# Performance work log

Hardware: AMD Instinct MI355X
Metric: run time of the kernel (lower is better)

The kernel has to match this reference:

```python
import jax, jax.numpy as jnp
import numpy as np

N, E, D, DE, H = 50000, 400000, 128, 64, 8
EPS = 1e-5
SLOPE = 0.2


def setup_inputs() -> dict:
    key = jax.random.key(0)
    ks = jax.random.split(key, 16)

    def lin(k, fan_in, fan_out):
        return (jax.random.normal(k, (fan_in, fan_out), jnp.float32) / np.sqrt(fan_in)).astype(jnp.float32)

    return {
        "node_features": jax.random.normal(ks[0], (N, D), jnp.float32),
        "edge_features": jax.random.normal(ks[1], (E, DE), jnp.float32),
        "Wn": lin(ks[2], D, D), "bn": jnp.zeros((D,), jnp.float32),
        "Wq": lin(ks[3], D, D), "bq": jnp.zeros((D,), jnp.float32),
        "Wk": lin(ks[4], D, D), "bk": jnp.zeros((D,), jnp.float32),
        "Wv": lin(ks[5], D, D), "bv": jnp.zeros((D,), jnp.float32),
        "We": lin(ks[6], DE, D), "be": jnp.zeros((D,), jnp.float32),
        "A1": lin(ks[7], 3 * D, D), "b1": jnp.zeros((D,), jnp.float32),
        "A2": lin(ks[8], D, H), "b2": jnp.zeros((H,), jnp.float32),
        "gamma": jnp.ones((D,), jnp.float32),
        "beta": jnp.zeros((D,), jnp.float32),
        "edge_index": jax.random.randint(ks[9], (2, E), 0, N, dtype=jnp.int32),
    }


def reference(node_features, edge_features, Wn, bn, Wq, bq, Wk, bk, Wv, bv,
              We, be, A1, b1, A2, b2, gamma, beta, edge_index):
    num_nodes = node_features.shape[0]
    h = node_features @ Wn + bn                      # [N, D]
    q = node_features @ Wq + bq                      # [N, D]
    k = node_features @ Wk + bk                      # [N, D]
    v = node_features @ Wv + bv                      # [N, D]
    eh = edge_features @ We + be                     # [E, D]

    src, tgt = edge_index[0], edge_index[1]
    attn_in = jnp.concatenate([q[src], k[tgt], eh], axis=-1)   # [E, 3D]
    hmid = jax.nn.leaky_relu(attn_in @ A1 + b1, SLOPE)          # [E, D]
    scores = jax.nn.leaky_relu(hmid @ A2 + b2, SLOPE)           # [E, H]
    w = jax.nn.softmax(scores.mean(axis=-1), axis=0)            # global softmax over edges, [E]

    # scatter-add: output[src] += w * v[tgt]
    out = jax.ops.segment_sum(w[:, None] * v[tgt], src, num_segments=num_nodes)  # [N, D]

    y = h + out                                       # dropout = identity (eval)
    mu = y.mean(axis=-1, keepdims=True)
    var = y.var(axis=-1, keepdims=True)
    return gamma * (y - mu) / jnp.sqrt(var + EPS) + beta
```

## Files before the change

### kernel.cpp

```cpp
#include <hip/hip_runtime.h>

#define D 128
#define DE 64
#define SLOPE 0.2f
#define EPS 1e-5f

typedef float f32x4 __attribute__((ext_vector_type(4)));
typedef short bf16x8 __attribute__((ext_vector_type(8)));
typedef unsigned short ushort;

__device__ __forceinline__ float lrelu(float x) { return x > 0.f ? x : SLOPE * x; }

__device__ __forceinline__ ushort f2bf(float x) {
  union { float f; unsigned u; } c; c.f = x;
  unsigned r = c.u + 0x7FFFu + ((c.u >> 16) & 1u);
  return (ushort)(r >> 16);
}
__device__ __forceinline__ float bf2f(unsigned u) {
  return __uint_as_float(u << 16);
}

__global__ __launch_bounds__(128) void fold_pack(
    const float* __restrict__ Wq, const float* __restrict__ Wk,
    const float* __restrict__ We, const float* __restrict__ A1,
    const float* __restrict__ bq, const float* __restrict__ bk,
    const float* __restrict__ be, const float* __restrict__ b1,
    const float* __restrict__ Wn, const float* __restrict__ Wv,
    ushort* __restrict__ AfqT, ushort* __restrict__ AfkT,
    ushort* __restrict__ AfeT, float* __restrict__ bfold,
    ushort* __restrict__ WnT, ushort* __restrict__ WvT) {
  int r = blockIdx.x;
  int j = threadIdx.x;
  if (r < 128) {
    float acc = 0.f;
    for (int t = 0; t < 128; ++t) acc += Wq[r * 128 + t] * A1[t * 128 + j];
    AfqT[j * 128 + r] = f2bf(acc);
  } else if (r < 256) {
    int k = r - 128;
    float acc = 0.f;
    for (int t = 0; t < 128; ++t) acc += Wk[k * 128 + t] * A1[(128 + t) * 128 + j];
    AfkT[j * 128 + k] = f2bf(acc);
  } else if (r < 320) {
    int k = r - 256;
    float acc = 0.f;
    for (int t = 0; t < 128; ++t) acc += We[k * 128 + t] * A1[(256 + t) * 128 + j];
    AfeT[j * 64 + k] = f2bf(acc);
  } else if (r == 320) {
    float acc = b1[j];
    for (int t = 0; t < 128; ++t) {
      acc += bq[t] * A1[t * 128 + j];
      acc += bk[t] * A1[(128 + t) * 128 + j];
      acc += be[t] * A1[(256 + t) * 128 + j];
    }
    bfold[j] = acc;
  } else if (r < 449) {
    int c = r - 321;
    WnT[c * 128 + j] = f2bf(Wn[j * 128 + c]);
  } else {
    int c = r - 449;
    WvT[c * 128 + j] = f2bf(Wv[j * 128 + c]);
  }
}

__global__ __launch_bounds__(256) void cvt_count(
    const float* __restrict__ X, ushort* __restrict__ Xb, int n4,
    const int* __restrict__ src, int* __restrict__ deg, int E) {
  int i = blockIdx.x * 256 + threadIdx.x;
  if (i < n4) {
    float4 f = ((const float4*)X)[i];
    union { ushort us[4]; uint2 v; } u;
    u.us[0] = f2bf(f.x); u.us[1] = f2bf(f.y);
    u.us[2] = f2bf(f.z); u.us[3] = f2bf(f.w);
    ((uint2*)Xb)[i] = u.v;
  }
  if (i < E) atomicAdd(&deg[src[i]], 1);
}

__global__ __launch_bounds__(256, 2) void node_gemm_mfma(
    const ushort* __restrict__ Xb, const ushort* __restrict__ WnT,
    const ushort* __restrict__ WvT, const ushort* __restrict__ AfqT,
    const ushort* __restrict__ AfkT, const float* __restrict__ bn,
    const float* __restrict__ bv, float* __restrict__ h,
    ushort* __restrict__ vb, ushort* __restrict__ q2p,
    ushort* __restrict__ k2p, int Nn) {
  __shared__ ushort As[256 * 40];
  __shared__ ushort Bs[128 * 40];
  __shared__ float bS[128];
  const ushort* WT;
  const float* bb = nullptr;
  float* O = nullptr;
  ushort* Ob = nullptr;
  int mode;
  switch (blockIdx.y) {
    case 0: WT = WnT; bb = bn; O = h; mode = 0; break;
    case 1: WT = WvT; bb = bv; Ob = vb; mode = 1; break;
    case 2: WT = AfqT; Ob = q2p; mode = 2; break;
    default: WT = AfkT; Ob = k2p; mode = 2; break;
  }
  const int t = threadIdx.x;
  if (t < 128) bS[t] = bb ? bb[t] : 0.f;
  const int seg = t & 3, arow = t >> 2;
  const int m0 = blockIdx.x * 256;
  int rIdx[4];
#pragma unroll
  for (int l = 0; l < 4; ++l) rIdx[l] = min(m0 + arow + 64 * l, Nn - 1);
  uint4 avA[4], avB[2];
#pragma unroll
  for (int l = 0; l < 4; ++l)
    avA[l] = *(const uint4*)(Xb + (size_t)rIdx[l] * 128 + seg * 8);
#pragma unroll
  for (int l = 0; l < 2; ++l)
    avB[l] = *(const uint4*)(WT + (arow + 64 * l) * 128 + seg * 8);
  f32x4 acc[4][8];
#pragma unroll
  for (int mt = 0; mt < 4; ++mt)
#pragma unroll
    for (int nt = 0; nt < 8; ++nt) acc[mt][nt] = (f32x4)(0.f);
  const int lane = t & 63, wv = t >> 6, l15 = lane & 15, quad = lane >> 4;
  for (int ch = 0; ch < 4; ++ch) {
#pragma unroll
    for (int l = 0; l < 4; ++l)
      *(uint4*)&As[(arow + 64 * l) * 40 + seg * 8] = avA[l];
#pragma unroll
    for (int l = 0; l < 2; ++l)
      *(uint4*)&Bs[(arow + 64 * l) * 40 + seg * 8] = avB[l];
    __syncthreads();
    if (ch < 3) {
      int o = (ch + 1) * 32 + seg * 8;
#pragma unroll
      for (int l = 0; l < 4; ++l)
        avA[l] = *(const uint4*)(Xb + (size_t)rIdx[l] * 128 + o);
#pragma unroll
      for (int l = 0; l < 2; ++l)
        avB[l] = *(const uint4*)(WT + (arow + 64 * l) * 128 + o);
    }
    bf16x8 af[4];
#pragma unroll
    for (int mt = 0; mt < 4; ++mt)
      af[mt] = *(const bf16x8*)&As[(wv * 64 + mt * 16 + l15) * 40 + quad * 8];
#pragma unroll
    for (int nt = 0; nt < 8; ++nt) {
      bf16x8 bfr = *(const bf16x8*)&Bs[(nt * 16 + l15) * 40 + quad * 8];
#pragma unroll
      for (int mt = 0; mt < 4; ++mt)
        acc[mt][nt] =
            __builtin_amdgcn_mfma_f32_16x16x32_bf16(af[mt], bfr, acc[mt][nt], 0, 0, 0);
    }
    __syncthreads();
  }
#pragma unroll
  for (int mt = 0; mt < 4; ++mt) {
    int rowb = m0 + wv * 64 + mt * 16 + quad * 4;
#pragma unroll
    for (int nt = 0; nt < 8; ++nt) {
      int col = nt * 16 + l15;
      float b = bS[col];
#pragma unroll
      for (int r = 0; r < 4; ++r) {
        int rg = rowb + r;
        if (rg < Nn) {
          if (mode == 0)      O[(size_t)rg * 128 + col] = acc[mt][nt][r] + b;
          else if (mode == 1) Ob[(size_t)rg * 128 + col] = f2bf(acc[mt][nt][r] + b);
          else                Ob[(size_t)rg * 128 + l15 * 8 + nt] = f2bf(acc[mt][nt][r]);
        }
      }
    }
  }
}

__global__ __launch_bounds__(256, 2) void edge_fused3(
    const float* __restrict__ EF, const ushort* __restrict__ AfeT,
    const float* __restrict__ bfold, const float* __restrict__ A2,
    const float* __restrict__ b2, const ushort* __restrict__ q2p,
    const ushort* __restrict__ k2p, const int* __restrict__ src,
    const int* __restrict__ tgt, float* __restrict__ s_out, int E) {
  __shared__ ushort As[256 * 40];
  __shared__ ushort Bs[128 * 40];
  __shared__ float A2s[128 * 9];
  __shared__ float bfS[128];
  __shared__ float b2s[8];
  const int t = threadIdx.x;
  const int e0 = blockIdx.x * 256;
  const int lane = t & 63, wv = t >> 6, l15 = lane & 15, quad = lane >> 4;

  int siA[16], tiA[16];
#pragma unroll
  for (int mt = 0; mt < 4; ++mt)
#pragma unroll
    for (int r = 0; r < 4; ++r) {
      int e = min(e0 + wv * 64 + mt * 16 + quad * 4 + r, E - 1);
      siA[mt * 4 + r] = src[e];
      tiA[mt * 4 + r] = tgt[e];
    }
  {
    if (t < 128) bfS[t] = bfold[t];
    if (t < 8) b2s[t] = b2[t];
#pragma unroll
    for (int l = 0; l < 4; ++l) {
      int i = t + l * 256;
      A2s[(i >> 3) * 9 + (i & 7)] = A2[i];
    }
  }
  const int seg = t & 3, arow = t >> 2;
  int ecl[4];
#pragma unroll
  for (int l = 0; l < 4; ++l) ecl[l] = min(e0 + arow + 64 * l, E - 1);
  uint4 avA[4], avB[2];
#pragma unroll
  for (int l = 0; l < 4; ++l) {
    const float* p = EF + (size_t)ecl[l] * 64 + seg * 8;
    float4 f0 = *(const float4*)p;
    float4 f1 = *(const float4*)(p + 4);
    union { ushort us[8]; uint4 v; } u;
    u.us[0] = f2bf(f0.x); u.us[1] = f2bf(f0.y);
    u.us[2] = f2bf(f0.z); u.us[3] = f2bf(f0.w);
    u.us[4] = f2bf(f1.x); u.us[5] = f2bf(f1.y);
    u.us[6] = f2bf(f1.z); u.us[7] = f2bf(f1.w);
    avA[l] = u.v;
  }
#pragma unroll
  for (int l = 0; l < 2; ++l)
    avB[l] = *(const uint4*)(AfeT + (arow + 64 * l) * 64 + seg * 8);
  f32x4 acc[4][8];
#pragma unroll
  for (int mt = 0; mt < 4; ++mt)
#pragma unroll
    for (int nt = 0; nt < 8; ++nt) acc[mt][nt] = (f32x4)(0.f);

#pragma unroll
  for (int ch = 0; ch < 2; ++ch) {
#pragma unroll
    for (int l = 0; l < 4; ++l)
      *(uint4*)&As[(arow + 64 * l) * 40 + seg * 8] = avA[l];
#pragma unroll
    for (int l = 0; l < 2; ++l)
      *(uint4*)&Bs[(arow + 64 * l) * 40 + seg * 8] = avB[l];
    __syncthreads();
    if (ch == 0) {
      int o = 32 + seg * 8;
#pragma unroll
      for (int l = 0; l < 4; ++l) {
        const float* p = EF + (size_t)ecl[l] * 64 + o;
        float4 f0 = *(const float4*)p;
        float4 f1 = *(const float4*)(p + 4);
        union { ushort us[8]; uint4 v; } u;
        u.us[0] = f2bf(f0.x); u.us[1] = f2bf(f0.y);
        u.us[2] = f2bf(f0.z); u.us[3] = f2bf(f0.w);
        u.us[4] = f2bf(f1.x); u.us[5] = f2bf(f1.y);
        u.us[6] = f2bf(f1.z); u.us[7] = f2bf(f1.w);
        avA[l] = u.v;
      }
#pragma unroll
      for (int l = 0; l < 2; ++l)
        avB[l] = *(const uint4*)(AfeT + (arow + 64 * l) * 64 + o);
    }
    bf16x8 af[4];
#pragma unroll
    for (int mt = 0; mt < 4; ++mt)
      af[mt] = *(const bf16x8*)&As[(wv * 64 + mt * 16 + l15) * 40 + quad * 8];
#pragma unroll
    for (int nt = 0; nt < 8; ++nt) {
      bf16x8 bfr = *(const bf16x8*)&Bs[(nt * 16 + l15) * 40 + quad * 8];
#pragma unroll
      for (int mt = 0; mt < 4; ++mt)
        acc[mt][nt] =
            __builtin_amdgcn_mfma_f32_16x16x32_bf16(af[mt], bfr, acc[mt][nt], 0, 0, 0);
    }
    if (ch == 0) __syncthreads();
  }

  float bfv[8];
#pragma unroll
  for (int nt = 0; nt < 8; ++nt) bfv[nt] = bfS[nt * 16 + l15];
  uint4 qv[2][4], kv[2][4];
#pragma unroll
  for (int r = 0; r < 4; ++r) {
    qv[0][r] = *(const uint4*)(q2p + (size_t)siA[r] * 128 + l15 * 8);
    kv[0][r] = *(const uint4*)(k2p + (size_t)tiA[r] * 128 + l15 * 8);
  }
#pragma unroll
  for (int mt = 0; mt < 4; ++mt) {
    int cur = mt & 1;
    if (mt < 3) {
#pragma unroll
      for (int r = 0; r < 4; ++r) {
        qv[cur ^ 1][r] = *(const uint4*)(q2p + (size_t)siA[(mt + 1) * 4 + r] * 128 + l15 * 8);
        kv[cur ^ 1][r] = *(const uint4*)(k2p + (size_t)tiA[(mt + 1) * 4 + r] * 128 + l15 * 8);
      }
    }
#pragma unroll
    for (int r = 0; r < 4; ++r) {
      const ushort* qs = (const ushort*)&qv[cur][r];
      const ushort* ks = (const ushort*)&kv[cur][r];
#pragma unroll
      for (int nt = 0; nt < 8; ++nt)
        acc[mt][nt][r] =
            lrelu(acc[mt][nt][r] + bf2f(qs[nt]) + bf2f(ks[nt]) + bfv[nt]);
    }
  }
  float tacc[4][4];
#pragma unroll
  for (int mt = 0; mt < 4; ++mt)
#pragma unroll
    for (int r = 0; r < 4; ++r) tacc[mt][r] = 0.f;
  for (int hh = 0; hh < 8; ++hh) {
    float a2v[8];
#pragma unroll
    for (int nt = 0; nt < 8; ++nt) a2v[nt] = A2s[nt * 144 + l15 * 9 + hh];
    float b2h = b2s[hh];
#pragma unroll
    for (int mt = 0; mt < 4; ++mt)
#pragma unroll
      for (int r = 0; r < 4; ++r) {
        float p = 0.f;
#pragma unroll
        for (int nt = 0; nt < 8; ++nt) p += acc[mt][nt][r] * a2v[nt];
        p += __shfl_xor(p, 1);
        p += __shfl_xor(p, 2);
        p += __shfl_xor(p, 4);
        p += __shfl_xor(p, 8);
        tacc[mt][r] += lrelu(p + b2h);
      }
  }
  if (l15 == 0) {
#pragma unroll
    for (int mt = 0; mt < 4; ++mt)
#pragma unroll
      for (int r = 0; r < 4; ++r) {
        int e = e0 + wv * 64 + mt * 16 + quad * 4 + r;
        if (e < E) s_out[e] = tacc[mt][r] * 0.125f;
      }
  }
}

__global__ __launch_bounds__(256) void softmax_partial(
    const float* __restrict__ s, int E, float2* __restrict__ part) {
  __shared__ float mS[256], sS[256];
  int tid = threadIdx.x;
  float m = -1e30f, sum = 0.f;
  for (int i = blockIdx.x * 256 + tid; i < E; i += gridDim.x * 256) {
    float x = s[i];
    if (x > m) {
      sum = sum * __expf(m - x) + 1.f;
      m = x;
    } else {
      sum += __expf(x - m);
    }
  }
  mS[tid] = m;
  sS[tid] = sum;
  __syncthreads();
  for (int off = 128; off > 0; off >>= 1) {
    if (tid < off) {
      float m1 = mS[tid], s1 = sS[tid];
      float m2 = mS[tid + off], s2 = sS[tid + off];
      float M = fmaxf(m1, m2);
      mS[tid] = M;
      sS[tid] = s1 * __expf(m1 - M) + s2 * __expf(m2 - M);
    }
    __syncthreads();
  }
  if (tid == 0) part[blockIdx.x] = make_float2(mS[0], sS[0]);
}

__global__ __launch_bounds__(256) void softmax_final(
    const float2* __restrict__ part, int nPart, float* __restrict__ MS) {
  __shared__ float mS[256], sS[256];
  int tid = threadIdx.x;
  float m = -1e30f, sum = 0.f;
  for (int i = tid; i < nPart; i += 256) {
    float2 p = part[i];
    float M = fmaxf(m, p.x);
    sum = sum * __expf(m - M) + p.y * __expf(p.x - M);
    m = M;
  }
  mS[tid] = m;
  sS[tid] = sum;
  __syncthreads();
  for (int off = 128; off > 0; off >>= 1) {
    if (tid < off) {
      float m1 = mS[tid], s1 = sS[tid];
      float m2 = mS[tid + off], s2 = sS[tid + off];
      float M = fmaxf(m1, m2);
      mS[tid] = M;
      sS[tid] = s1 * __expf(m1 - M) + s2 * __expf(m2 - M);
    }
    __syncthreads();
  }
  if (tid == 0) {
    MS[0] = mS[0];
    MS[1] = 1.f / sS[0];
  }
}

__global__ __launch_bounds__(256) void scan1(const int* __restrict__ deg,
                                             int* __restrict__ incl,
                                             int* __restrict__ bsum, int N) {
  __shared__ int sh[256];
  int tid = threadIdx.x;
  int i = blockIdx.x * 256 + tid;
  sh[tid] = (i < N) ? deg[i] : 0;
  __syncthreads();
  for (int off = 1; off < 256; off <<= 1) {
    int tv = (tid >= off) ? sh[tid - off] : 0;
    __syncthreads();
    sh[tid] += tv;
    __syncthreads();
  }
  if (i < N) incl[i] = sh[tid];
  if (tid == 255) bsum[blockIdx.x] = sh[255];
}

__global__ __launch_bounds__(256) void scan2(int* __restrict__ bsum, int nb) {
  __shared__ int sh[256];
  int tid = threadIdx.x;
  sh[tid] = (tid < nb) ? bsum[tid] : 0;
  __syncthreads();
  for (int off = 1; off < 256; off <<= 1) {
    int tv = (tid >= off) ? sh[tid - off] : 0;
    __syncthreads();
    sh[tid] += tv;
    __syncthreads();
  }
  if (tid < nb) bsum[tid] = sh[tid];
}

__global__ __launch_bounds__(256) void scan3(const int* __restrict__ deg,
                                             const int* __restrict__ incl,
                                             const int* __restrict__ bsum,
                                             int* __restrict__ offs,
                                             int* __restrict__ cursor, int N,
                                             int E) {
  int i = blockIdx.x * 256 + threadIdx.x;
  if (i >= N) return;
  int base = (blockIdx.x > 0) ? bsum[blockIdx.x - 1] : 0;
  int ex = incl[i] - deg[i] + base;
  offs[i] = ex;
  cursor[i] = ex;
  if (i == N - 1) offs[N] = E;
}

__global__ __launch_bounds__(256) void fill_csr(
    const int* __restrict__ src, const int* __restrict__ tgt,
    const float* __restrict__ s, int* __restrict__ cursor,
    int2* __restrict__ cwt, int E) {
  int e = blockIdx.x * 256 + threadIdx.x;
  if (e >= E) return;
  int s_ = src[e];
  int j = atomicAdd(&cursor[s_], 1);
  cwt[j] = make_int2(tgt[e], __float_as_int(s[e]));
}

__global__ __launch_bounds__(256) void gather_ln(
    const int* __restrict__ offs, const int2* __restrict__ cwt,
    const ushort* __restrict__ vb, const float* __restrict__ MS,
    const float* __restrict__ gamma, const float* __restrict__ beta,
    float* __restrict__ y, int N) {
  int tid = threadIdx.x;
  int n = blockIdx.x * 4 + (tid >> 6);
  if (n >= N) return;
  int lane = tid & 63;
  float M = MS[0], inv = MS[1];
  int beg = offs[n], end = offs[n + 1];
  float a0 = 0.f, a1 = 0.f;
  int j = beg;
  for (; j + 1 < end; j += 2) {
    int2 p0 = cwt[j], p1 = cwt[j + 1];
    float w0 = __expf(__int_as_float(p0.y) - M) * inv;
    float w1 = __expf(__int_as_float(p1.y) - M) * inv;
    unsigned u0 = *(const unsigned*)(vb + (size_t)p0.x * 128 + lane * 2);
    unsigned u1 = *(const unsigned*)(vb + (size_t)p1.x * 128 + lane * 2);
    a0 += w0 * bf2f(u0 & 0xffffu) + w1 * bf2f(u1 & 0xffffu);
    a1 += w0 * bf2f(u0 >> 16) + w1 * bf2f(u1 >> 16);
  }
  if (j < end) {
    int2 p = cwt[j];
    float w = __expf(__int_as_float(p.y) - M) * inv;
    unsigned u = *(const unsigned*)(vb + (size_t)p.x * 128 + lane * 2);
    a0 += w * bf2f(u & 0xffffu);
    a1 += w * bf2f(u >> 16);
  }
  size_t base = (size_t)n * 128 + lane * 2;
  float2 hv = *(const float2*)(y + base);
  float y0 = hv.x + a0, y1 = hv.y + a1;
  float sum = y0 + y1, ssq = y0 * y0 + y1 * y1;
#pragma unroll
  for (int off = 1; off < 64; off <<= 1) {
    sum += __shfl_xor(sum, off);
    ssq += __shfl_xor(ssq, off);
  }
  float mu = sum * (1.f / 128.f);
  float var = ssq * (1.f / 128.f) - mu * mu;
  float rstd = rsqrtf(var + EPS);
  float2 g = *(const float2*)(gamma + lane * 2);
  float2 bt = *(const float2*)(beta + lane * 2);
  float2 out;
  out.x = g.x * (y0 - mu) * rstd + bt.x;
  out.y = g.y * (y1 - mu) * rstd + bt.y;
  *(float2*)(y + base) = out;
}

extern "C" void kernel_launch(void* const* d_in, const int* in_sizes, int n_in,
                              void* d_out, int out_size, void* d_ws,
                              size_t ws_size, hipStream_t stream) {
  const float* X  = (const float*)d_in[0];
  const float* EF = (const float*)d_in[1];
  const float* Wn = (const float*)d_in[2];
  const float* bn = (const float*)d_in[3];
  const float* Wq = (const float*)d_in[4];
  const float* bq = (const float*)d_in[5];
  const float* Wk = (const float*)d_in[6];
  const float* bk = (const float*)d_in[7];
  const float* Wv = (const float*)d_in[8];
  const float* bv = (const float*)d_in[9];
  const float* We = (const float*)d_in[10];
  const float* be = (const float*)d_in[11];
  const float* A1 = (const float*)d_in[12];
  const float* b1 = (const float*)d_in[13];
  const float* A2 = (const float*)d_in[14];
  const float* b2 = (const float*)d_in[15];
  const float* gamma = (const float*)d_in[16];
  const float* beta  = (const float*)d_in[17];
  const int* ei = (const int*)d_in[18];

  int N = in_sizes[0] / D;
  int E = in_sizes[1] / DE;
  const int* src = ei;
  const int* tgt = ei + E;

  float* h = (float*)d_out;
  float* ws = (float*)d_ws;
  float* sbuf  = ws;
  float2* part = (float2*)(sbuf + E);
  float* MS    = (float*)(part + 1024);
  float* bfold = MS + 4;
  ushort* Xb   = (ushort*)(bfold + 128);
  ushort* vb   = Xb + (size_t)N * D;
  ushort* q2p  = vb + (size_t)N * D;
  ushort* k2p  = q2p + (size_t)N * D;
  ushort* AfqT = k2p + (size_t)N * D;
  ushort* AfkT = AfqT + 128 * 128;
  ushort* AfeT = AfkT + 128 * 128;
  ushort* WnT  = AfeT + 128 * 64;
  ushort* WvT  = WnT + 128 * 128;
  int* deg    = (int*)(WvT + 128 * 128);
  int* incl   = deg + N;
  int* bsum   = incl + N;
  int* cursor = bsum + 256;
  int* offs   = cursor + N;
  int2* cwt   = (int2*)(offs + N + 2);

  int nbScan = (N + 255) / 256;
  int n4 = N * D / 4;

  hipMemsetAsync(deg, 0, (size_t)N * sizeof(int), stream);
  fold_pack<<<577, 128, 0, stream>>>(Wq, Wk, We, A1, bq, bk, be, b1, Wn, Wv,
                                     AfqT, AfkT, AfeT, bfold, WnT, WvT);
  cvt_count<<<(n4 + 255) / 256, 256, 0, stream>>>(X, Xb, n4, src, deg, E);
  scan1<<<nbScan, 256, 0, stream>>>(deg, incl, bsum, N);
  scan2<<<1, 256, 0, stream>>>(bsum, nbScan);
  scan3<<<nbScan, 256, 0, stream>>>(deg, incl, bsum, offs, cursor, N, E);
  node_gemm_mfma<<<dim3((N + 255) / 256, 4), 256, 0, stream>>>(
      Xb, WnT, WvT, AfqT, AfkT, bn, bv, h, vb, q2p, k2p, N);
  edge_fused3<<<(E + 255) / 256, 256, 0, stream>>>(EF, AfeT, bfold, A2, b2,
                                                   q2p, k2p, src, tgt, sbuf, E);
  softmax_partial<<<1024, 256, 0, stream>>>(sbuf, E, part);
  softmax_final<<<1, 256, 0, stream>>>(part, 1024, MS);
  fill_csr<<<(E + 255) / 256, 256, 0, stream>>>(src, tgt, sbuf, cursor, cwt, E);
  gather_ln<<<(N + 3) / 4, 256, 0, stream>>>(offs, cwt, vb, MS, gamma, beta, h,
                                             N);
}
```

Measured before the change: 457.3 us.

## Fuse X conversion into node GEMM and softmax/CSR fill into edge kernel

After: 384.6 us. 1.19x faster.

```diff
diff --git a/kernel.cpp b/kernel.cpp
--- a/kernel.cpp
+++ b/kernel.cpp
@@ -18,6 +18,16 @@
 }
 __device__ __forceinline__ float bf2f(unsigned u) {
   return __uint_as_float(u << 16);
+}
+__device__ __forceinline__ uint4 cvt8(const float* p) {
+  float4 f0 = *(const float4*)p;
+  float4 f1 = *(const float4*)(p + 4);
+  union { ushort us[8]; uint4 v; } u;
+  u.us[0] = f2bf(f0.x); u.us[1] = f2bf(f0.y);
+  u.us[2] = f2bf(f0.z); u.us[3] = f2bf(f0.w);
+  u.us[4] = f2bf(f1.x); u.us[5] = f2bf(f1.y);
+  u.us[6] = f2bf(f1.z); u.us[7] = f2bf(f1.w);
+  return u.v;
 }
 
 __global__ __launch_bounds__(128) void fold_pack(
@@ -28,7 +38,8 @@
     const float* __restrict__ Wn, const float* __restrict__ Wv,
     ushort* __restrict__ AfqT, ushort* __restrict__ AfkT,
     ushort* __restrict__ AfeT, float* __restrict__ bfold,
-    ushort* __restrict__ WnT, ushort* __restrict__ WvT) {
+    ushort* __restrict__ WnT, ushort* __restrict__ WvT,
+    const int* __restrict__ src, int* __restrict__ deg, int E) {
   int r = blockIdx.x;
   int j = threadIdx.x;
   if (r < 128) {
@@ -56,28 +67,17 @@
   } else if (r < 449) {
     int c = r - 321;
     WnT[c * 128 + j] = f2bf(Wn[j * 128 + c]);
-  } else {
+  } else if (r < 577) {
     int c = r - 449;
     WvT[c * 128 + j] = f2bf(Wv[j * 128 + c]);
-  }
-}
-
-__global__ __launch_bounds__(256) void cvt_count(
-    const float* __restrict__ X, ushort* __restrict__ Xb, int n4,
-    const int* __restrict__ src, int* __restrict__ deg, int E) {
-  int i = blockIdx.x * 256 + threadIdx.x;
-  if (i < n4) {
-    float4 f = ((const float4*)X)[i];
-    union { ushort us[4]; uint2 v; } u;
-    u.us[0] = f2bf(f.x); u.us[1] = f2bf(f.y);
-    u.us[2] = f2bf(f.z); u.us[3] = f2bf(f.w);
-    ((uint2*)Xb)[i] = u.v;
-  }
-  if (i < E) atomicAdd(&deg[src[i]], 1);
+  } else {
+    int i = (r - 577) * 128 + j;
+    if (i < E) atomicAdd(&deg[src[i]], 1);
+  }
 }
 
 __global__ __launch_bounds__(256, 2) void node_gemm_mfma(
-    const ushort* __restrict__ Xb, const ushort* __restrict__ WnT,
+    const float* __restrict__ X, const ushort* __restrict__ WnT,
     const ushort* __restrict__ WvT, const ushort* __restrict__ AfqT,
     const ushort* __restrict__ AfkT, const float* __restrict__ bn,
     const float* __restrict__ bv, float* __restrict__ h,
@@ -107,7 +107,7 @@
   uint4 avA[4], avB[2];
 #pragma unroll
   for (int l = 0; l < 4; ++l)
-    avA[l] = *(const uint4*)(Xb + (size_t)rIdx[l] * 128 + seg * 8);
+    avA[l] = cvt8(X + (size_t)rIdx[l] * 128 + seg * 8);
 #pragma unroll
   for (int l = 0; l < 2; ++l)
     avB[l] = *(const uint4*)(WT + (arow + 64 * l) * 128 + seg * 8);
@@ -129,7 +129,7 @@
       int o = (ch + 1) * 32 + seg * 8;
 #pragma unroll
       for (int l = 0; l < 4; ++l)
-        avA[l] = *(const uint4*)(Xb + (size_t)rIdx[l] * 128 + o);
+        avA[l] = cvt8(X + (size_t)rIdx[l] * 128 + o);
 #pragma unroll
       for (int l = 0; l < 2; ++l)
         avB[l] = *(const uint4*)(WT + (arow + 64 * l) * 128 + o);
@@ -168,101 +168,76 @@
   }
 }
 
-__global__ __launch_bounds__(256, 2) void edge_fused3(
+__global__ __launch_bounds__(256, 3) void edge_fused4(
     const float* __restrict__ EF, const ushort* __restrict__ AfeT,
     const float* __restrict__ bfold, const float* __restrict__ A2,
     const float* __restrict__ b2, const ushort* __restrict__ q2p,
     const ushort* __restrict__ k2p, const int* __restrict__ src,
-    const int* __restrict__ tgt, float* __restrict__ s_out, int E) {
-  __shared__ ushort As[256 * 40];
+    const int* __restrict__ tgt, int* __restrict__ cursor,
+    int2* __restrict__ cwt, float2* __restrict__ part, int E) {
+  __shared__ ushort As[128 * 40];
   __shared__ ushort Bs[128 * 40];
   __shared__ float A2s[128 * 9];
   __shared__ float bfS[128];
   __shared__ float b2s[8];
+  __shared__ int sIdxS[128], sIdxT[128];
+  __shared__ float redM[16], redS[16];
   const int t = threadIdx.x;
-  const int e0 = blockIdx.x * 256;
+  const int e0 = blockIdx.x * 128;
+  if (t < 128) {
+    sIdxS[t] = src[min(e0 + t, E - 1)];
+    bfS[t] = bfold[t];
+  } else {
+    sIdxT[t - 128] = tgt[min(e0 + t - 128, E - 1)];
+  }
+  if (t < 8) b2s[t] = b2[t];
+#pragma unroll
+  for (int l = 0; l < 4; ++l) {
+    int i = t + l * 256;
+    A2s[(i >> 3) * 9 + (i & 7)] = A2[i];
+  }
+  const int seg = t & 3, arow = t >> 2;
+  int ecl[2];
+#pragma unroll
+  for (int l = 0; l < 2; ++l) ecl[l] = min(e0 + arow + 64 * l, E - 1);
+  uint4 avA[2], avB[2];
+#pragma unroll
+  for (int l = 0; l < 2; ++l) {
+    avA[l] = cvt8(EF + (size_t)ecl[l] * 64 + seg * 8);
+    avB[l] = *(const uint4*)(AfeT + (arow + 64 * l) * 64 + seg * 8);
+  }
+  f32x4 acc[2][8];
+#pragma unroll
+  for (int mt = 0; mt < 2; ++mt)
+#pragma unroll
+    for (int nt = 0; nt < 8; ++nt) acc[mt][nt] = (f32x4)(0.f);
   const int lane = t & 63, wv = t >> 6, l15 = lane & 15, quad = lane >> 4;
 
-  int siA[16], tiA[16];
-#pragma unroll
-  for (int mt = 0; mt < 4; ++mt)
-#pragma unroll
-    for (int r = 0; r < 4; ++r) {
-      int e = min(e0 + wv * 64 + mt * 16 + quad * 4 + r, E - 1);
-      siA[mt * 4 + r] = src[e];
-      tiA[mt * 4 + r] = tgt[e];
-    }
-  {
-    if (t < 128) bfS[t] = bfold[t];
-    if (t < 8) b2s[t] = b2[t];
-#pragma unroll
-    for (int l = 0; l < 4; ++l) {
-      int i = t + l * 256;
-      A2s[(i >> 3) * 9 + (i & 7)] = A2[i];
-    }
-  }
-  const int seg = t & 3, arow = t >> 2;
-  int ecl[4];
-#pragma unroll
-  for (int l = 0; l < 4; ++l) ecl[l] = min(e0 + arow + 64 * l, E - 1);
-  uint4 avA[4], avB[2];
-#pragma unroll
-  for (int l = 0; l < 4; ++l) {
-    const float* p = EF + (size_t)ecl[l] * 64 + seg * 8;
-    float4 f0 = *(const float4*)p;
-    float4 f1 = *(const float4*)(p + 4);
-    union { ushort us[8]; uint4 v; } u;
-    u.us[0] = f2bf(f0.x); u.us[1] = f2bf(f0.y);
-    u.us[2] = f2bf(f0.z); u.us[3] = f2bf(f0.w);
-    u.us[4] = f2bf(f1.x); u.us[5] = f2bf(f1.y);
-    u.us[6] = f2bf(f1.z); u.us[7] = f2bf(f1.w);
-    avA[l] = u.v;
-  }
-#pragma unroll
-  for (int l = 0; l < 2; ++l)
-    avB[l] = *(const uint4*)(AfeT + (arow + 64 * l) * 64 + seg * 8);
-  f32x4 acc[4][8];
-#pragma unroll
-  for (int mt = 0; mt < 4; ++mt)
-#pragma unroll
-    for (int nt = 0; nt < 8; ++nt) acc[mt][nt] = (f32x4)(0.f);
-
 #pragma unroll
   for (int ch = 0; ch < 2; ++ch) {
 #pragma unroll
-    for (int l = 0; l < 4; ++l)
+    for (int l = 0; l < 2; ++l) {
       *(uint4*)&As[(arow + 64 * l) * 40 + seg * 8] = avA[l];
-#pragma unroll
-    for (int l = 0; l < 2; ++l)
       *(uint4*)&Bs[(arow + 64 * l) * 40 + seg * 8] = avB[l];
+    }
     __syncthreads();
     if (ch == 0) {
       int o = 32 + seg * 8;
 #pragma unroll
-      for (int l = 0; l < 4; ++l) {
-        const float* p = EF + (size_t)ecl[l] * 64 + o;
-        float4 f0 = *(const float4*)p;
-        float4 f1 = *(const float4*)(p + 4);
-        union { ushort us[8]; uint4 v; } u;
-        u.us[0] = f2bf(f0.x); u.us[1] = f2bf(f0.y);
-        u.us[2] = f2bf(f0.z); u.us[3] = f2bf(f0.w);
-        u.us[4] = f2bf(f1.x); u.us[5] = f2bf(f1.y);
-        u.us[6] = f2bf(f1.z); u.us[7] = f2bf(f1.w);
-        avA[l] = u.v;
+      for (int l = 0; l < 2; ++l) {
+        avA[l] = cvt8(EF + (size_t)ecl[l] * 64 + o);
+        avB[l] = *(const uint4*)(AfeT + (arow + 64 * l) * 64 + o);
       }
-#pragma unroll
-      for (int l = 0; l < 2; ++l)
-        avB[l] = *(const uint4*)(AfeT + (arow + 64 * l) * 64 + o);
-    }
-    bf16x8 af[4];
-#pragma unroll
-    for (int mt = 0; mt < 4; ++mt)
-      af[mt] = *(const bf16x8*)&As[(wv * 64 + mt * 16 + l15) * 40 + quad * 8];
+    }
+    bf16x8 af[2];
+#pragma unroll
+    for (int mt = 0; mt < 2; ++mt)
+      af[mt] = *(const bf16x8*)&As[(wv * 32 + mt * 16 + l15) * 40 + quad * 8];
 #pragma unroll
     for (int nt = 0; nt < 8; ++nt) {
       bf16x8 bfr = *(const bf16x8*)&Bs[(nt * 16 + l15) * 40 + quad * 8];
 #pragma unroll
-      for (int mt = 0; mt < 4; ++mt)
+      for (int mt = 0; mt < 2; ++mt)
         acc[mt][nt] =
             __builtin_amdgcn_mfma_f32_16x16x32_bf16(af[mt], bfr, acc[mt][nt], 0, 0, 0);
     }
@@ -272,35 +247,25 @@
   float bfv[8];
 #pragma unroll
   for (int nt = 0; nt < 8; ++nt) bfv[nt] = bfS[nt * 16 + l15];
-  uint4 qv[2][4], kv[2][4];
-#pragma unroll
-  for (int r = 0; r < 4; ++r) {
-    qv[0][r] = *(const uint4*)(q2p + (size_t)siA[r] * 128 + l15 * 8);
-    kv[0][r] = *(const uint4*)(k2p + (size_t)tiA[r] * 128 + l15 * 8);
-  }
-#pragma unroll
-  for (int mt = 0; mt < 4; ++mt) {
-    int cur = mt & 1;
-    if (mt < 3) {
-#pragma unroll
-      for (int r = 0; r < 4; ++r) {
-        qv[cur ^ 1][r] = *(const uint4*)(q2p + (size_t)siA[(mt + 1) * 4 + r] * 128 + l15 * 8);
-        kv[cur ^ 1][r] = *(const uint4*)(k2p + (size_t)tiA[(mt + 1) * 4 + r] * 128 + l15 * 8);
-      }
-    }
+#pragma unroll
+  for (int mt = 0; mt < 2; ++mt) {
 #pragma unroll
     for (int r = 0; r < 4; ++r) {
-      const ushort* qs = (const ushort*)&qv[cur][r];
-      const ushort* ks = (const ushort*)&kv[cur][r];
+      int erow = wv * 32 + mt * 16 + quad * 4 + r;
+      int si = sIdxS[erow], ti = sIdxT[erow];
+      uint4 qv = *(const uint4*)(q2p + (size_t)si * 128 + l15 * 8);
+      uint4 kv = *(const uint4*)(k2p + (size_t)ti * 128 + l15 * 8);
+      const ushort* qs = (const ushort*)&qv;
+      const ushort* ks = (const ushort*)&kv;
 #pragma unroll
       for (int nt = 0; nt < 8; ++nt)
         acc[mt][nt][r] =
             lrelu(acc[mt][nt][r] + bf2f(qs[nt]) + bf2f(ks[nt]) + bfv[nt]);
     }
   }
-  float tacc[4][4];
-#pragma unroll
-  for (int mt = 0; mt < 4; ++mt)
+  float tacc[2][4];
+#pragma unroll
+  for (int mt = 0; mt < 2; ++mt)
 #pragma unroll
     for (int r = 0; r < 4; ++r) tacc[mt][r] = 0.f;
   for (int hh = 0; hh < 8; ++hh) {
@@ -309,7 +274,7 @@
     for (int nt = 0; nt < 8; ++nt) a2v[nt] = A2s[nt * 144 + l15 * 9 + hh];
     float b2h = b2s[hh];
 #pragma unroll
-    for (int mt = 0; mt < 4; ++mt)
+    for (int mt = 0; mt < 2; ++mt)
 #pragma unroll
       for (int r = 0; r < 4; ++r) {
         float p = 0.f;
@@ -323,44 +288,46 @@
       }
   }
   if (l15 == 0) {
-#pragma unroll
-    for (int mt = 0; mt < 4; ++mt)
+    float sc[8];
+    float m = -1e30f;
+#pragma unroll
+    for (int mt = 0; mt < 2; ++mt)
 #pragma unroll
       for (int r = 0; r < 4; ++r) {
-        int e = e0 + wv * 64 + mt * 16 + quad * 4 + r;
-        if (e < E) s_out[e] = tacc[mt][r] * 0.125f;
+        int i = mt * 4 + r;
+        sc[i] = tacc[mt][r] * 0.125f;
+        int e = e0 + wv * 32 + mt * 16 + quad * 4 + r;
+        if (e < E) m = fmaxf(m, sc[i]);
       }
-  }
-}
-
-__global__ __launch_bounds__(256) void softmax_partial(
-    const float* __restrict__ s, int E, float2* __restrict__ part) {
-  __shared__ float mS[256], sS[256];
-  int tid = threadIdx.x;
-  float m = -1e30f, sum = 0.f;
-  for (int i = blockIdx.x * 256 + tid; i < E; i += gridDim.x * 256) {
-    float x = s[i];
-    if (x > m) {
-      sum = sum * __expf(m - x) + 1.f;
-      m = x;
-    } else {
-      sum += __expf(x - m);
-    }
-  }
-  mS[tid] = m;
-  sS[tid] = sum;
+    float ssum = 0.f;
+#pragma unroll
+    for (int mt = 0; mt < 2; ++mt)
+#pragma unroll
+      for (int r = 0; r < 4; ++r) {
+        int i = mt * 4 + r;
+        int erow = wv * 32 + mt * 16 + quad * 4 + r;
+        if (e0 + erow < E) {
+          ssum += __expf(sc[i] - m);
+          int j = atomicAdd(&cursor[sIdxS[erow]], 1);
+          cwt[j] = make_int2(sIdxT[erow], __float_as_int(sc[i]));
+        }
+      }
+    int rid = wv * 4 + quad;
+    redM[rid] = m;
+    redS[rid] = ssum;
+  }
   __syncthreads();
-  for (int off = 128; off > 0; off >>= 1) {
-    if (tid < off) {
-      float m1 = mS[tid], s1 = sS[tid];
-      float m2 = mS[tid + off], s2 = sS[tid + off];
-      float M = fmaxf(m1, m2);
-      mS[tid] = M;
-      sS[tid] = s1 * __expf(m1 - M) + s2 * __expf(m2 - M);
-    }
-    __syncthreads();
-  }
-  if (tid == 0) part[blockIdx.x] = make_float2(mS[0], sS[0]);
+  if (t == 0) {
+    float M = redM[0], S = redS[0];
+#pragma unroll
+    for (int i = 1; i < 16; ++i) {
+      float m2 = redM[i], s2 = redS[i];
+      float Mn = fmaxf(M, m2);
+      S = S * __expf(M - Mn) + s2 * __expf(m2 - Mn);
+      M = Mn;
+    }
+    part[blockIdx.x] = make_float2(M, S);
+  }
 }
 
 __global__ __launch_bounds__(256) void softmax_final(
@@ -440,17 +407,6 @@
   if (i == N - 1) offs[N] = E;
 }
 
-__global__ __launch_bounds__(256) void fill_csr(
-    const int* __restrict__ src, const int* __restrict__ tgt,
-    const float* __restrict__ s, int* __restrict__ cursor,
-    int2* __restrict__ cwt, int E) {
-  int e = blockIdx.x * 256 + threadIdx.x;
-  if (e >= E) return;
-  int s_ = src[e];
-  int j = atomicAdd(&cursor[s_], 1);
-  cwt[j] = make_int2(tgt[e], __float_as_int(s[e]));
-}
-
 __global__ __launch_bounds__(256) void gather_ln(
     const int* __restrict__ offs, const int2* __restrict__ cwt,
     const ushort* __restrict__ vb, const float* __restrict__ MS,
@@ -464,16 +420,22 @@
   int beg = offs[n], end = offs[n + 1];
   float a0 = 0.f, a1 = 0.f;
   int j = beg;
-  for (; j + 1 < end; j += 2) {
-    int2 p0 = cwt[j], p1 = cwt[j + 1];
+  for (; j + 4 <= end; j += 4) {
+    int2 p0 = cwt[j], p1 = cwt[j + 1], p2 = cwt[j + 2], p3 = cwt[j + 3];
+    unsigned u0 = *(const unsigned*)(vb + (size_t)p0.x * 128 + lane * 2);
+    unsigned u1 = *(const unsigned*)(vb + (size_t)p1.x * 128 + lane * 2);
+    unsigned u2 = *(const unsigned*)(vb + (size_t)p2.x * 128 + lane * 2);
+    unsigned u3 = *(const unsigned*)(vb + (size_t)p3.x * 128 + lane * 2);
     float w0 = __expf(__int_as_float(p0.y) - M) * inv;
     float w1 = __expf(__int_as_float(p1.y) - M) * inv;
-    unsigned u0 = *(const unsigned*)(vb + (size_t)p0.x * 128 + lane * 2);
-    unsigned u1 = *(const unsigned*)(vb + (size_t)p1.x * 128 + lane * 2);
-    a0 += w0 * bf2f(u0 & 0xffffu) + w1 * bf2f(u1 & 0xffffu);
-    a1 += w0 * bf2f(u0 >> 16) + w1 * bf2f(u1 >> 16);
-  }
-  if (j < end) {
+    float w2 = __expf(__int_as_float(p2.y) - M) * inv;
+    float w3 = __expf(__int_as_float(p3.y) - M) * inv;
+    a0 += w0 * bf2f(u0 & 0xffffu) + w1 * bf2f(u1 & 0xffffu) +
+          w2 * bf2f(u2 & 0xffffu) + w3 * bf2f(u3 & 0xffffu);
+    a1 += w0 * bf2f(u0 >> 16) + w1 * bf2f(u1 >> 16) + w2 * bf2f(u2 >> 16) +
+          w3 * bf2f(u3 >> 16);
+  }
+  for (; j < end; ++j) {
     int2 p = cwt[j];
     float w = __expf(__int_as_float(p.y) - M) * inv;
     unsigned u = *(const unsigned*)(vb + (size_t)p.x * 128 + lane * 2);
@@ -530,12 +492,10 @@
 
   float* h = (float*)d_out;
   float* ws = (float*)d_ws;
-  float* sbuf  = ws;
-  float2* part = (float2*)(sbuf + E);
-  float* MS    = (float*)(part + 1024);
+  float2* part = (float2*)ws;
+  float* MS    = (float*)(part + 4096);
   float* bfold = MS + 4;
-  ushort* Xb   = (ushort*)(bfold + 128);
-  ushort* vb   = Xb + (size_t)N * D;
+  ushort* vb   = (ushort*)(bfold + 128);
   ushort* q2p  = vb + (size_t)N * D;
   ushort* k2p  = q2p + (size_t)N * D;
   ushort* AfqT = k2p + (size_t)N * D;
@@ -551,22 +511,21 @@
   int2* cwt   = (int2*)(offs + N + 2);
 
   int nbScan = (N + 255) / 256;
-  int n4 = N * D / 4;
+  int nbEdge = (E + 127) / 128;
+  int nbHist = (E + 127) / 128;
 
   hipMemsetAsync(deg, 0, (size_t)N * sizeof(int), stream);
-  fold_pack<<<577, 128, 0, stream>>>(Wq, Wk, We, A1, bq, bk, be, b1, Wn, Wv,
-                                     AfqT, AfkT, AfeT, bfold, WnT, WvT);
-  cvt_count<<<(n4 + 255) / 256, 256, 0, stream>>>(X, Xb, n4, src, deg, E);
+  fold_pack<<<577 + nbHist, 128, 0, stream>>>(Wq, Wk, We, A1, bq, bk, be, b1,
+                                              Wn, Wv, AfqT, AfkT, AfeT, bfold,
+                                              WnT, WvT, src, deg, E);
   scan1<<<nbScan, 256, 0, stream>>>(deg, incl, bsum, N);
   scan2<<<1, 256, 0, stream>>>(bsum, nbScan);
   scan3<<<nbScan, 256, 0, stream>>>(deg, incl, bsum, offs, cursor, N, E);
   node_gemm_mfma<<<dim3((N + 255) / 256, 4), 256, 0, stream>>>(
-      Xb, WnT, WvT, AfqT, AfkT, bn, bv, h, vb, q2p, k2p, N);
-  edge_fused3<<<(E + 255) / 256, 256, 0, stream>>>(EF, AfeT, bfold, A2, b2,
-                                                   q2p, k2p, src, tgt, sbuf, E);
-  softmax_partial<<<1024, 256, 0, stream>>>(sbuf, E, part);
-  softmax_final<<<1, 256, 0, stream>>>(part, 1024, MS);
-  fill_csr<<<(E + 255) / 256, 256, 0, stream>>>(src, tgt, sbuf, cursor, cwt, E);
+      X, WnT, WvT, AfqT, AfkT, bn, bv, h, vb, q2p, k2p, N);
+  edge_fused4<<<nbEdge, 256, 0, stream>>>(EF, AfeT, bfold, A2, b2, q2p, k2p,
+                                          src, tgt, cursor, cwt, part, E);
+  softmax_final<<<1, 256, 0, stream>>>(part, nbEdge, MS);
   gather_ln<<<(N + 3) / 4, 256, 0, stream>>>(offs, cwt, vb, MS, gamma, beta, h,
                                              N);
 }
```
